# Optimization experiments

Hardware: AMD Instinct MI355X
Metric: run time of the kernel (lower is better)

Reference implementation:

```python
import jax, jax.numpy as jnp
import numpy as np
import math


def setup_inputs() -> dict:
    key = jax.random.key(0)
    k_x, k_q, k_k, k_v, k_o = jax.random.split(key, 5)
    B, S, D_IN, H, D_K, D_V, D_OUT = 1, 4096, 512, 8, 64, 64, 512
    # torch.rand -> uniform[0,1); scaled by 0.02 to keep softmax unsaturated
    scale = 0.02
    return {
        "x": jax.random.normal(k_x, (B, S, D_IN), dtype=jnp.float32),
        "W_q": jax.random.uniform(k_q, (H, D_IN, D_K), dtype=jnp.float32) * scale,
        "W_k": jax.random.uniform(k_k, (H, D_IN, D_K), dtype=jnp.float32) * scale,
        "W_v": jax.random.uniform(k_v, (H, D_IN, D_V), dtype=jnp.float32) * scale,
        "W_o": jax.random.uniform(k_o, (H, D_V, D_OUT), dtype=jnp.float32) * scale,
    }


def reference(x, W_q, W_k, W_v, W_o):
    # x: [B,S,d_in]; W_q/W_k: [H,d_in,d_k]; W_v: [H,d_in,d_v]; W_o: [H,d_v,d_out]
    S = x.shape[-2]
    d_key = W_k.shape[-1]
    Q = jnp.einsum('hjk,blj->bhlk', W_q, x)   # [B,H,S,d_k]
    K = jnp.einsum('hjk,blj->bhlk', W_k, x)   # [B,H,S,d_k]
    V = jnp.einsum('hjk,blj->bhlk', W_v, x)   # [B,H,S,d_v]
    # causal mask: True where masked (strict upper triangle)
    mask = jnp.triu(jnp.ones((S, S), dtype=bool), k=1)  # [S,S]
    scores = jnp.einsum('bhik,bhjk->bhij', Q, K)        # [B,H,S,S]
    scores = jnp.where(mask, -jnp.inf, scores)
    # is_scaled=True: divide by sqrt(d_key) before softmax
    weights = jax.nn.softmax(scores / math.sqrt(d_key), axis=-1)
    weights = jnp.where(mask, 0.0, weights)
    values = jnp.einsum('bhij,bhjv->bhiv', weights, V)  # [B,H,S,d_v]
    return jnp.einsum('hvk,bhlv->blk', W_o, values)     # [B,S,d_out]
```

## Files before the change

kernel.cpp:

```cpp
#include <hip/hip_runtime.h>
#include <hip/hip_bf16.h>
#include <math.h>

#define S_LEN 4096
#define NH    8

typedef __attribute__((ext_vector_type(8))) short bf16x8;
typedef __attribute__((ext_vector_type(4))) short bf16x4;
typedef __attribute__((ext_vector_type(4))) float f32x4;
typedef __attribute__((ext_vector_type(16))) float f32x16;
typedef __attribute__((ext_vector_type(2)))  int   int32x2;
typedef __attribute__((ext_vector_type(4)))  unsigned short u16x4;

#define QSCALE 0.18033688011112042f

#define WAIT_VM6 0x0F76
#define WAIT_VM4 0x0F74
#define WAIT_VM0 0x0F70

__device__ __forceinline__ short f2bf(float f) {
    union { float f; unsigned u; } v; v.f = f;
    unsigned r = v.u + 0x7fffu + ((v.u >> 16) & 1u);
    return (short)(r >> 16);
}

__device__ __forceinline__ float bf2f(unsigned short s) {
    union { unsigned u; float f; } v; v.u = ((unsigned)s) << 16; return v.f;
}

__device__ __forceinline__ int pk2(float a, float b) {
    __hip_bfloat162 t = __float22bfloat162_rn(make_float2(a, b));
    union { __hip_bfloat162 h; int i; } u; u.h = t;
    return u.i;
}

__device__ __forceinline__ void gload16(const void* g, void* l) {
    __builtin_amdgcn_global_load_lds(
        (const __attribute__((address_space(1))) unsigned*)g,
        (__attribute__((address_space(3))) unsigned*)l, 16, 0, 0);
}

__device__ __forceinline__ void stage_tile(const short* gsrc, size_t gstride,
                                           short* tile, int t)
{
    const int wave = t >> 6, lane = t & 63;
    const int sub = lane >> 3;
    const int cg  = (lane & 7) ^ sub;
#pragma unroll
    for (int j = 0; j < 2; ++j) {
        const int chunk = wave * 2 + j;
        const int row = chunk * 8 + sub;
        gload16(gsrc + (size_t)row * gstride + cg * 8, tile + chunk * 512);
    }
}

__device__ __forceinline__ bf16x8 frag(const short* tile, int row, int cg) {
    return *(const bf16x8*)&tile[row * 64 + ((cg ^ (row & 7)) << 3)];
}

__device__ __forceinline__ bf16x8 mk_bp(const f32x16& sc, const int p, float& lsum)
{
    const float e0 = __builtin_amdgcn_exp2f(sc[8 * p + 0]);
    const float e1 = __builtin_amdgcn_exp2f(sc[8 * p + 1]);
    const float e2 = __builtin_amdgcn_exp2f(sc[8 * p + 2]);
    const float e3 = __builtin_amdgcn_exp2f(sc[8 * p + 3]);
    const float e4 = __builtin_amdgcn_exp2f(sc[8 * p + 4]);
    const float e5 = __builtin_amdgcn_exp2f(sc[8 * p + 5]);
    const float e6 = __builtin_amdgcn_exp2f(sc[8 * p + 6]);
    const float e7 = __builtin_amdgcn_exp2f(sc[8 * p + 7]);
    lsum += ((e0 + e1) + (e2 + e3)) + ((e4 + e5) + (e6 + e7));
    int we0 = pk2(e0, e1), we1 = pk2(e2, e3);
    int wo0 = pk2(e4, e5), wo1 = pk2(e6, e7);
    const int32x2 r0 = __builtin_amdgcn_permlane32_swap(we0, wo0, false, false);
    const int32x2 r1 = __builtin_amdgcn_permlane32_swap(we1, wo1, false, false);
    union { int i[4]; bf16x8 v; } u;
    u.i[0] = r0[0]; u.i[1] = r1[0]; u.i[2] = r0[1]; u.i[3] = r1[1];
    return u.v;
}

__device__ __forceinline__ void gemm_mainloop_512(
    const short* __restrict__ Arow, const short* __restrict__ Brow,
    short* As, short* Bs, f32x4 acc[4], int t)
{
    const int wave = t >> 6, lane = t & 63, n16 = lane & 15, quad = lane >> 4;
    stage_tile(Arow, 512, As, t);
    stage_tile(Brow, 512, Bs, t);
    for (int c = 0; c < 8; ++c) {
        const int cur = c & 1;
        __builtin_amdgcn_s_barrier();
        if (c < 7) {
            stage_tile(Arow + (c + 1) * 64, 512, As + (1 - cur) * 4096, t);
            stage_tile(Brow + (c + 1) * 64, 512, Bs + (1 - cur) * 4096, t);
            __builtin_amdgcn_s_waitcnt(WAIT_VM4);
        } else {
            __builtin_amdgcn_s_waitcnt(WAIT_VM0);
        }
        __builtin_amdgcn_s_barrier();
        const short* as = As + cur * 4096;
        const short* bs = Bs + cur * 4096;
#pragma unroll
        for (int kh = 0; kh < 2; ++kh) {
            const bf16x8 a = frag(as, wave * 16 + n16, kh * 4 + quad);
#pragma unroll
            for (int nt = 0; nt < 4; ++nt) {
                const bf16x8 b = frag(bs, nt * 16 + n16, kh * 4 + quad);
                acc[nt] = __builtin_amdgcn_mfma_f32_16x16x32_bf16(a, b, acc[nt], 0, 0, 0);
            }
        }
    }
}

__global__ __launch_bounds__(256) void prep_kernel(
    const float* __restrict__ x,
    const float* __restrict__ Wq, const float* __restrict__ Wk,
    const float* __restrict__ Wv, const float* __restrict__ Wo,
    short* __restrict__ xb, short* __restrict__ Wqkvt, short* __restrict__ Wot)
{
    __shared__ short T[64 * 66];
    const int b = blockIdx.x, t = threadIdx.x;
    if (b < 1024) {
        const size_t idx = (size_t)b * 2048 + t * 8;
        const float4 a = *(const float4*)&x[idx];
        const float4 c = *(const float4*)&x[idx + 4];
        bf16x8 o;
        o[0] = f2bf(a.x); o[1] = f2bf(a.y); o[2] = f2bf(a.z); o[3] = f2bf(a.w);
        o[4] = f2bf(c.x); o[5] = f2bf(c.y); o[6] = f2bf(c.z); o[7] = f2bf(c.w);
        *(bf16x8*)&xb[idx] = o;
        return;
    }
    const int c4 = (t & 15) * 4, rsub = t >> 4;
    const int orow = t >> 2, oc16 = (t & 3) * 16;
    if (b < 1216) {
        const int jj = b - 1024, g = jj >> 3, kb = jj & 7;
        const int which = g >> 3, h = g & 7;
        const float* W = ((which == 0) ? Wq : (which == 1) ? Wk : Wv) + (size_t)h * 512 * 64;
#pragma unroll
        for (int p = 0; p < 4; ++p) {
            const int row = p * 16 + rsub;
            const float4 v = *(const float4*)&W[(size_t)(kb * 64 + row) * 64 + c4];
            T[(c4 + 0) * 66 + row] = f2bf(v.x);
            T[(c4 + 1) * 66 + row] = f2bf(v.y);
            T[(c4 + 2) * 66 + row] = f2bf(v.z);
            T[(c4 + 3) * 66 + row] = f2bf(v.w);
        }
        __syncthreads();
        short* O = &Wqkvt[((size_t)g * 64 + orow) * 512 + kb * 64];
        *(bf16x8*)&O[oc16]     = *(const bf16x8*)&T[orow * 66 + oc16];
        *(bf16x8*)&O[oc16 + 8] = *(const bf16x8*)&T[orow * 66 + oc16 + 8];
    } else {
        const int jj = b - 1216, h = jj >> 3, nb = jj & 7;
        const float* W = Wo + (size_t)h * 64 * 512;
#pragma unroll
        for (int p = 0; p < 4; ++p) {
            const int row = p * 16 + rsub;
            const float4 v = *(const float4*)&W[(size_t)row * 512 + nb * 64 + c4];
            T[(c4 + 0) * 66 + row] = f2bf(v.x);
            T[(c4 + 1) * 66 + row] = f2bf(v.y);
            T[(c4 + 2) * 66 + row] = f2bf(v.z);
            T[(c4 + 3) * 66 + row] = f2bf(v.w);
        }
        __syncthreads();
        short* O = &Wot[((size_t)nb * 64 + orow) * 512 + h * 64];
        *(bf16x8*)&O[oc16]     = *(const bf16x8*)&T[orow * 66 + oc16];
        *(bf16x8*)&O[oc16 + 8] = *(const bf16x8*)&T[orow * 66 + oc16 + 8];
    }
}

__global__ __launch_bounds__(256) void qkv_gemm_kernel(
    const short* __restrict__ xb, const short* __restrict__ Wqkvt,
    short* __restrict__ Qg, short* __restrict__ Kg, short* __restrict__ Vtg)
{
    __shared__ short smem[24576];
    short* As = smem;
    short* Bs = smem + 16384;
    const int sblk = blockIdx.x, g = blockIdx.y;
    const int which = g >> 3, h = g & 7;
    const int t = threadIdx.x;
    const int wave = t >> 6, lane = t & 63, n16 = lane & 15, quad = lane >> 4;

    const short* Arow = xb + (size_t)sblk * 128 * 512;
    const short* Brow = Wqkvt + (size_t)g * 64 * 512;

    f32x4 acc[2][4] = {{{0,0,0,0},{0,0,0,0},{0,0,0,0},{0,0,0,0}},
                       {{0,0,0,0},{0,0,0,0},{0,0,0,0},{0,0,0,0}}};

    stage_tile(Arow,            512, As,        t);
    stage_tile(Arow + 64 * 512, 512, As + 4096, t);
    stage_tile(Brow,            512, Bs,        t);
    for (int c = 0; c < 8; ++c) {
        const int cur = c & 1;
        __builtin_amdgcn_s_barrier();
        if (c < 7) {
            stage_tile(Arow + (c + 1) * 64,            512, As + (1 - cur) * 8192,        t);
            stage_tile(Arow + 64 * 512 + (c + 1) * 64, 512, As + (1 - cur) * 8192 + 4096, t);
            stage_tile(Brow + (c + 1) * 64,            512, Bs + (1 - cur) * 4096,        t);
            __builtin_amdgcn_s_waitcnt(WAIT_VM6);
        } else {
            __builtin_amdgcn_s_waitcnt(WAIT_VM0);
        }
        __builtin_amdgcn_s_barrier();
        const short* as = As + cur * 8192;
        const short* bs = Bs + cur * 4096;
        const int r0 = wave * 32 + n16;
        const short* a_sub = as + (r0 >> 6) * 4096;
#pragma unroll
        for (int kh = 0; kh < 2; ++kh) {
            const bf16x8 a0 = frag(a_sub, r0 & 63,        kh * 4 + quad);
            const bf16x8 a1 = frag(a_sub, (r0 & 63) + 16, kh * 4 + quad);
#pragma unroll
            for (int nt = 0; nt < 4; ++nt) {
                const bf16x8 b = frag(bs, nt * 16 + n16, kh * 4 + quad);
                acc[0][nt] = __builtin_amdgcn_mfma_f32_16x16x32_bf16(a0, b, acc[0][nt], 0, 0, 0);
                acc[1][nt] = __builtin_amdgcn_mfma_f32_16x16x32_bf16(a1, b, acc[1][nt], 0, 0, 0);
            }
        }
    }

    if (which < 2) {
        const float scale = (which == 0) ? QSCALE : 1.0f;
        short* O = ((which == 0) ? Qg : Kg) + (size_t)h * S_LEN * 64;
#pragma unroll
        for (int m = 0; m < 2; ++m)
#pragma unroll
            for (int nt = 0; nt < 4; ++nt)
#pragma unroll
                for (int r = 0; r < 4; ++r) {
                    const int s = sblk * 128 + wave * 32 + m * 16 + quad * 4 + r;
                    O[(size_t)s * 64 + nt * 16 + n16] = f2bf(acc[m][nt][r] * scale);
                }
    } else {
        __syncthreads();
        short* Tr = smem;
#pragma unroll
        for (int m = 0; m < 2; ++m)
#pragma unroll
            for (int nt = 0; nt < 4; ++nt)
#pragma unroll
                for (int r = 0; r < 4; ++r)
                    Tr[(nt * 16 + n16) * 130 + wave * 32 + m * 16 + quad * 4 + r] =
                        f2bf(acc[m][nt][r]);
        __syncthreads();
        short* O = Vtg + (size_t)h * 64 * S_LEN + sblk * 128;
        const int vr = t >> 2, c32 = (t & 3) * 32;
#pragma unroll
        for (int u = 0; u < 4; ++u)
            *(bf16x8*)&O[(size_t)vr * S_LEN + c32 + u * 8] =
                *(const bf16x8*)&Tr[vr * 130 + c32 + u * 8];
    }
}

__global__ __launch_bounds__(256) void out_gemm_kernel(
    const short* __restrict__ vals, const short* __restrict__ Wot, float* __restrict__ out)
{
    __shared__ short smem[16384];
    short* As = smem;
    short* Bs = smem + 8192;
    const int sblk = blockIdx.x, g = blockIdx.y;
    const int t = threadIdx.x;
    const int wave = t >> 6, lane = t & 63, n16 = lane & 15, quad = lane >> 4;

    f32x4 acc[4] = {{0,0,0,0},{0,0,0,0},{0,0,0,0},{0,0,0,0}};
    gemm_mainloop_512(vals + (size_t)sblk * 64 * 512, Wot + (size_t)g * 64 * 512,
                      As, Bs, acc, t);

#pragma unroll
    for (int nt = 0; nt < 4; ++nt)
#pragma unroll
        for (int r = 0; r < 4; ++r) {
            const int s = sblk * 64 + wave * 16 + quad * 4 + r;
            out[(size_t)s * 512 + g * 64 + nt * 16 + n16] = acc[nt][r];
        }
}

__global__ __launch_bounds__(256, 3) void attn_kernel(
    const short* __restrict__ Qg, const short* __restrict__ Kg,
    const short* __restrict__ Vtg, short* __restrict__ Opart, float* __restrict__ Lpart)
{
    __shared__ short Ks[2][4096];
    __shared__ short Vs[2][4096];

    const int id = blockIdx.x;
    const int h  = id & 7;
    const int c  = 79 - (id >> 3);
    int qs, j;
    if (c < 8)       { qs = c;                   j = 0; }
    else if (c < 24) { qs = 8 + ((c - 8) >> 1);  j = (c - 8) & 1; }
    else if (c < 48) { qs = 16 + (c - 24) / 3;   j = (c - 24) % 3; }
    else             { qs = 24 + ((c - 48) >> 2); j = (c - 48) & 3; }
    const int k0   = j * 16;
    const int kend = min(k0 + 16, 2 * qs + 2);

    const short* Kh  = Kg  + (size_t)h * S_LEN * 64;
    const short* Vth = Vtg + (size_t)h * 64 * S_LEN;

    const int t = threadIdx.x;
    const int wave = t >> 6, lane = t & 63, l31 = lane & 31, half = lane >> 5;
    const int qg = qs * 128 + wave * 32 + l31;

    const short* Qr = Qg + (size_t)h * S_LEN * 64 + (size_t)qg * 64;
    bf16x8 bq[4];
#pragma unroll
    for (int kc = 0; kc < 4; ++kc)
        bq[kc] = *(const bf16x8*)&Qr[kc * 16 + half * 8];

    f32x16 z16;
#pragma unroll
    for (int r = 0; r < 16; ++r) z16[r] = 0.f;

    f32x16 oacc[2];
#pragma unroll
    for (int r = 0; r < 16; ++r) { oacc[0][r] = 0.f; oacc[1][r] = 0.f; }
    float llane = 0.f;

    stage_tile(Kh + (size_t)k0 * 64 * 64, 64, Ks[0], t);
    stage_tile(Vth + k0 * 64, S_LEN, Vs[0], t);

    for (int kb = k0; kb < kend; ++kb) {
        const int cur = (kb - k0) & 1;
        __builtin_amdgcn_s_barrier();
        if (kb + 1 < kend) {
            stage_tile(Kh + (size_t)(kb + 1) * 64 * 64, 64, Ks[1 - cur], t);
            stage_tile(Vth + (kb + 1) * 64, S_LEN, Vs[1 - cur], t);
            __builtin_amdgcn_s_waitcnt(WAIT_VM4);
        } else {
            __builtin_amdgcn_s_waitcnt(WAIT_VM0);
        }
        __builtin_amdgcn_s_barrier();

        __builtin_amdgcn_s_setprio(1);
        f32x16 sc0, sc1;
        {
            const bf16x8 a0 = frag(Ks[cur], l31,      half);
            const bf16x8 a1 = frag(Ks[cur], 32 + l31, half);
            sc0 = __builtin_amdgcn_mfma_f32_32x32x16_bf16(a0, bq[0], z16, 0, 0, 0);
            sc1 = __builtin_amdgcn_mfma_f32_32x32x16_bf16(a1, bq[0], z16, 0, 0, 0);
        }
#pragma unroll
        for (int kc = 1; kc < 4; ++kc) {
            const bf16x8 a0 = frag(Ks[cur], l31,      kc * 2 + half);
            const bf16x8 a1 = frag(Ks[cur], 32 + l31, kc * 2 + half);
            sc0 = __builtin_amdgcn_mfma_f32_32x32x16_bf16(a0, bq[kc], sc0, 0, 0, 0);
            sc1 = __builtin_amdgcn_mfma_f32_32x32x16_bf16(a1, bq[kc], sc1, 0, 0, 0);
        }
        __builtin_amdgcn_s_setprio(0);

        if (kb * 64 + 63 > qg) {
#pragma unroll
            for (int r = 0; r < 16; ++r) {
                const int keyb = kb * 64 + (r & 3) + 8 * (r >> 2) + 4 * half;
                if (keyb > qg)      sc0[r] = -1e30f;
                if (keyb + 32 > qg) sc1[r] = -1e30f;
            }
        }

        bf16x8 bp[4];
        bp[0] = mk_bp(sc0, 0, llane);
        bp[1] = mk_bp(sc0, 1, llane);
        bp[2] = mk_bp(sc1, 0, llane);
        bp[3] = mk_bp(sc1, 1, llane);

        __builtin_amdgcn_s_setprio(1);
#pragma unroll
        for (int kc = 0; kc < 4; ++kc) {
            const bf16x8 a0 = frag(Vs[cur], l31,      kc * 2 + half);
            const bf16x8 a1 = frag(Vs[cur], 32 + l31, kc * 2 + half);
            oacc[0] = __builtin_amdgcn_mfma_f32_32x32x16_bf16(a0, bp[kc], oacc[0], 0, 0, 0);
            oacc[1] = __builtin_amdgcn_mfma_f32_32x32x16_bf16(a1, bp[kc], oacc[1], 0, 0, 0);
        }
        __builtin_amdgcn_s_setprio(0);
    }

    short* tileO = Opart + (size_t)(h * 80 + c) * (64 * 128);
    float* tileL = Lpart + (h * 80 + c) * 128;
    const float lq = llane + __shfl_xor(llane, 32, 64);
    if (half == 0) tileL[wave * 32 + l31] = lq;
#pragma unroll
    for (int mt = 0; mt < 2; ++mt)
#pragma unroll
        for (int r = 0; r < 16; ++r) {
            const int v = mt * 32 + (r & 3) + 8 * (r >> 2) + 4 * half;
            tileO[(v << 7) + wave * 32 + l31] = f2bf(mt ? oacc[1][r] : oacc[0][r]);
        }
}

__global__ __launch_bounds__(256) void combine_norm_kernel(
    const short* __restrict__ Opart, const float* __restrict__ Lpart,
    short* __restrict__ vals)
{
    __shared__ short T[128 * 66];
    const int id = blockIdx.x;
    const int h = id & 7, qs = id >> 3;
    int c0, nj;
    if (qs < 8)       { c0 = qs;                 nj = 1; }
    else if (qs < 16) { c0 = 8 + 2 * (qs - 8);   nj = 2; }
    else if (qs < 24) { c0 = 24 + 3 * (qs - 16); nj = 3; }
    else              { c0 = 48 + 4 * (qs - 24); nj = 4; }
    const int base = h * 80 + c0;

    const int t = threadIdx.x;
    const int q0 = (t & 31) * 4;
    const int vr = t >> 5;

    f32x4 L = {0, 0, 0, 0};
    for (int j = 0; j < nj; ++j)
        L += *(const f32x4*)&Lpart[(base + j) * 128 + q0];
    const f32x4 inv = {1.f / L[0], 1.f / L[1], 1.f / L[2], 1.f / L[3]};

#pragma unroll
    for (int pass = 0; pass < 8; ++pass) {
        const int v = vr + pass * 8;
        f32x4 s = {0, 0, 0, 0};
        for (int j = 0; j < nj; ++j) {
            const u16x4 u = *(const u16x4*)&Opart[(size_t)(base + j) * 8192 + (v << 7) + q0];
            s[0] += bf2f(u[0]); s[1] += bf2f(u[1]);
            s[2] += bf2f(u[2]); s[3] += bf2f(u[3]);
        }
        T[(q0 + 0) * 66 + v] = f2bf(s[0] * inv[0]);
        T[(q0 + 1) * 66 + v] = f2bf(s[1] * inv[1]);
        T[(q0 + 2) * 66 + v] = f2bf(s[2] * inv[2]);
        T[(q0 + 3) * 66 + v] = f2bf(s[3] * inv[3]);
    }
    __syncthreads();
    const int q = t >> 1, vh = (t & 1) * 32;
    const size_t row = (size_t)(qs * 128 + q) * 512 + h * 64 + vh;
#pragma unroll
    for (int u = 0; u < 4; ++u)
        *(bf16x8*)&vals[row + u * 8] = *(const bf16x8*)&T[q * 66 + vh + u * 8];
}

extern "C" void kernel_launch(void* const* d_in, const int* in_sizes, int n_in,
                              void* d_out, int out_size, void* d_ws, size_t ws_size,
                              hipStream_t stream)
{
    const float* x  = (const float*)d_in[0];
    const float* Wq = (const float*)d_in[1];
    const float* Wk = (const float*)d_in[2];
    const float* Wv = (const float*)d_in[3];
    const float* Wo = (const float*)d_in[4];
    float* out = (float*)d_out;

    short* xb    = (short*)d_ws;
    short* Wqkvt = xb + 2097152;
    short* Wot   = Wqkvt + 786432;
    short* Qg    = Wot + 262144;
    short* Kg    = Qg + 2097152;
    short* Vtg   = Kg + 2097152;
    short* vals  = Vtg + 2097152;
    short* Opart = vals + 2097152;
    float* Lpart = (float*)(Opart + (size_t)640 * 8192);

    prep_kernel<<<1280, 256, 0, stream>>>(x, Wq, Wk, Wv, Wo, xb, Wqkvt, Wot);
    qkv_gemm_kernel<<<dim3(32, 24), 256, 0, stream>>>(xb, Wqkvt, Qg, Kg, Vtg);
    attn_kernel<<<640, 256, 0, stream>>>(Qg, Kg, Vtg, Opart, Lpart);
    combine_norm_kernel<<<256, 256, 0, stream>>>(Opart, Lpart, vals);
    out_gemm_kernel<<<dim3(64, 8), 256, 0, stream>>>(vals, Wot, out);
}
```

Before: 135.2 us.

## Fuse all five stages into one cooperative persistent kernel with grid syncs

Folds the prep, QKV GEMM, attention, combine and output GEMM stages into one cooperative kernel of 768 blocks, separated by grid-wide barriers. If the cooperative launch fails it falls back to the original five launches. The aim is to remove four kernel launch gaps and tails. In exchange, every stage now runs with the fused kernel's register and occupancy limits (launch_bounds 256,3), and grid.sync adds its own barrier cost.

```diff
diff --git a/kernel.cpp b/kernel.cpp
--- a/kernel.cpp
+++ b/kernel.cpp
@@ -1,4 +1,5 @@
 #include <hip/hip_runtime.h>
+#include <hip/hip_cooperative_groups.h>
 #include <hip/hip_bf16.h>
 #include <math.h>
 
@@ -110,14 +111,13 @@
     }
 }
 
-__global__ __launch_bounds__(256) void prep_kernel(
+__device__ __forceinline__ void prep_body(
+    int b, int t, short* T,
     const float* __restrict__ x,
     const float* __restrict__ Wq, const float* __restrict__ Wk,
     const float* __restrict__ Wv, const float* __restrict__ Wo,
     short* __restrict__ xb, short* __restrict__ Wqkvt, short* __restrict__ Wot)
 {
-    __shared__ short T[64 * 66];
-    const int b = blockIdx.x, t = threadIdx.x;
     if (b < 1024) {
         const size_t idx = (size_t)b * 2048 + t * 8;
         const float4 a = *(const float4*)&x[idx];
@@ -166,16 +166,14 @@
     }
 }
 
-__global__ __launch_bounds__(256) void qkv_gemm_kernel(
+__device__ __forceinline__ void qkv_body(
+    int sblk, int g, int t, short* smem,
     const short* __restrict__ xb, const short* __restrict__ Wqkvt,
     short* __restrict__ Qg, short* __restrict__ Kg, short* __restrict__ Vtg)
 {
-    __shared__ short smem[24576];
     short* As = smem;
     short* Bs = smem + 16384;
-    const int sblk = blockIdx.x, g = blockIdx.y;
     const int which = g >> 3, h = g & 7;
-    const int t = threadIdx.x;
     const int wave = t >> 6, lane = t & 63, n16 = lane & 15, quad = lane >> 4;
 
     const short* Arow = xb + (size_t)sblk * 128 * 512;
@@ -249,37 +247,12 @@
     }
 }
 
-__global__ __launch_bounds__(256) void out_gemm_kernel(
-    const short* __restrict__ vals, const short* __restrict__ Wot, float* __restrict__ out)
-{
-    __shared__ short smem[16384];
-    short* As = smem;
-    short* Bs = smem + 8192;
-    const int sblk = blockIdx.x, g = blockIdx.y;
-    const int t = threadIdx.x;
-    const int wave = t >> 6, lane = t & 63, n16 = lane & 15, quad = lane >> 4;
-
-    f32x4 acc[4] = {{0,0,0,0},{0,0,0,0},{0,0,0,0},{0,0,0,0}};
-    gemm_mainloop_512(vals + (size_t)sblk * 64 * 512, Wot + (size_t)g * 64 * 512,
-                      As, Bs, acc, t);
-
-#pragma unroll
-    for (int nt = 0; nt < 4; ++nt)
-#pragma unroll
-        for (int r = 0; r < 4; ++r) {
-            const int s = sblk * 64 + wave * 16 + quad * 4 + r;
-            out[(size_t)s * 512 + g * 64 + nt * 16 + n16] = acc[nt][r];
-        }
-}
-
-__global__ __launch_bounds__(256, 3) void attn_kernel(
+__device__ __forceinline__ void attn_body(
+    int id, int t, short* smem,
     const short* __restrict__ Qg, const short* __restrict__ Kg,
-    const short* __restrict__ Vtg, short* __restrict__ Opart, float* __restrict__ Lpart)
-{
-    __shared__ short Ks[2][4096];
-    __shared__ short Vs[2][4096];
-
-    const int id = blockIdx.x;
+    const short* __restrict__ Vtg, short* __restrict__ Opart,
+    float* __restrict__ Lpart)
+{
     const int h  = id & 7;
     const int c  = 79 - (id >> 3);
     int qs, j;
@@ -293,7 +266,6 @@
     const short* Kh  = Kg  + (size_t)h * S_LEN * 64;
     const short* Vth = Vtg + (size_t)h * 64 * S_LEN;
 
-    const int t = threadIdx.x;
     const int wave = t >> 6, lane = t & 63, l31 = lane & 31, half = lane >> 5;
     const int qg = qs * 128 + wave * 32 + l31;
 
@@ -312,15 +284,17 @@
     for (int r = 0; r < 16; ++r) { oacc[0][r] = 0.f; oacc[1][r] = 0.f; }
     float llane = 0.f;
 
-    stage_tile(Kh + (size_t)k0 * 64 * 64, 64, Ks[0], t);
-    stage_tile(Vth + k0 * 64, S_LEN, Vs[0], t);
+    stage_tile(Kh + (size_t)k0 * 64 * 64, 64, smem, t);
+    stage_tile(Vth + k0 * 64, S_LEN, smem + 8192, t);
 
     for (int kb = k0; kb < kend; ++kb) {
         const int cur = (kb - k0) & 1;
+        const short* Kc = smem + cur * 4096;
+        const short* Vc = smem + 8192 + cur * 4096;
         __builtin_amdgcn_s_barrier();
         if (kb + 1 < kend) {
-            stage_tile(Kh + (size_t)(kb + 1) * 64 * 64, 64, Ks[1 - cur], t);
-            stage_tile(Vth + (kb + 1) * 64, S_LEN, Vs[1 - cur], t);
+            stage_tile(Kh + (size_t)(kb + 1) * 64 * 64, 64, smem + (1 - cur) * 4096, t);
+            stage_tile(Vth + (kb + 1) * 64, S_LEN, smem + 8192 + (1 - cur) * 4096, t);
             __builtin_amdgcn_s_waitcnt(WAIT_VM4);
         } else {
             __builtin_amdgcn_s_waitcnt(WAIT_VM0);
@@ -330,15 +304,15 @@
         __builtin_amdgcn_s_setprio(1);
         f32x16 sc0, sc1;
         {
-            const bf16x8 a0 = frag(Ks[cur], l31,      half);
-            const bf16x8 a1 = frag(Ks[cur], 32 + l31, half);
+            const bf16x8 a0 = frag(Kc, l31,      half);
+            const bf16x8 a1 = frag(Kc, 32 + l31, half);
             sc0 = __builtin_amdgcn_mfma_f32_32x32x16_bf16(a0, bq[0], z16, 0, 0, 0);
             sc1 = __builtin_amdgcn_mfma_f32_32x32x16_bf16(a1, bq[0], z16, 0, 0, 0);
         }
 #pragma unroll
         for (int kc = 1; kc < 4; ++kc) {
-            const bf16x8 a0 = frag(Ks[cur], l31,      kc * 2 + half);
-            const bf16x8 a1 = frag(Ks[cur], 32 + l31, kc * 2 + half);
+            const bf16x8 a0 = frag(Kc, l31,      kc * 2 + half);
+            const bf16x8 a1 = frag(Kc, 32 + l31, kc * 2 + half);
             sc0 = __builtin_amdgcn_mfma_f32_32x32x16_bf16(a0, bq[kc], sc0, 0, 0, 0);
             sc1 = __builtin_amdgcn_mfma_f32_32x32x16_bf16(a1, bq[kc], sc1, 0, 0, 0);
         }
@@ -362,8 +336,8 @@
         __builtin_amdgcn_s_setprio(1);
 #pragma unroll
         for (int kc = 0; kc < 4; ++kc) {
-            const bf16x8 a0 = frag(Vs[cur], l31,      kc * 2 + half);
-            const bf16x8 a1 = frag(Vs[cur], 32 + l31, kc * 2 + half);
+            const bf16x8 a0 = frag(Vc, l31,      kc * 2 + half);
+            const bf16x8 a1 = frag(Vc, 32 + l31, kc * 2 + half);
             oacc[0] = __builtin_amdgcn_mfma_f32_32x32x16_bf16(a0, bp[kc], oacc[0], 0, 0, 0);
             oacc[1] = __builtin_amdgcn_mfma_f32_32x32x16_bf16(a1, bp[kc], oacc[1], 0, 0, 0);
         }
@@ -383,12 +357,11 @@
         }
 }
 
-__global__ __launch_bounds__(256) void combine_norm_kernel(
+__device__ __forceinline__ void combine_body(
+    int id, int t, short* T,
     const short* __restrict__ Opart, const float* __restrict__ Lpart,
     short* __restrict__ vals)
 {
-    __shared__ short T[128 * 66];
-    const int id = blockIdx.x;
     const int h = id & 7, qs = id >> 3;
     int c0, nj;
     if (qs < 8)       { c0 = qs;                 nj = 1; }
@@ -397,7 +370,6 @@
     else              { c0 = 48 + 4 * (qs - 24); nj = 4; }
     const int base = h * 80 + c0;
 
-    const int t = threadIdx.x;
     const int q0 = (t & 31) * 4;
     const int vr = t >> 5;
 
@@ -426,6 +398,98 @@
 #pragma unroll
     for (int u = 0; u < 4; ++u)
         *(bf16x8*)&vals[row + u * 8] = *(const bf16x8*)&T[q * 66 + vh + u * 8];
+}
+
+__device__ __forceinline__ void out_body(
+    int sblk, int g, int t, short* smem,
+    const short* __restrict__ vals, const short* __restrict__ Wot,
+    float* __restrict__ out)
+{
+    short* As = smem;
+    short* Bs = smem + 8192;
+    const int wave = t >> 6, lane = t & 63, n16 = lane & 15, quad = lane >> 4;
+
+    f32x4 acc[4] = {{0,0,0,0},{0,0,0,0},{0,0,0,0},{0,0,0,0}};
+    gemm_mainloop_512(vals + (size_t)sblk * 64 * 512, Wot + (size_t)g * 64 * 512,
+                      As, Bs, acc, t);
+
+#pragma unroll
+    for (int nt = 0; nt < 4; ++nt)
+#pragma unroll
+        for (int r = 0; r < 4; ++r) {
+            const int s = sblk * 64 + wave * 16 + quad * 4 + r;
+            out[(size_t)s * 512 + g * 64 + nt * 16 + n16] = acc[nt][r];
+        }
+}
+
+__global__ __launch_bounds__(256, 3) void fused_kernel(
+    const float* __restrict__ x,
+    const float* __restrict__ Wq, const float* __restrict__ Wk,
+    const float* __restrict__ Wv, const float* __restrict__ Wo,
+    float* __restrict__ out,
+    short* __restrict__ xb, short* __restrict__ Wqkvt, short* __restrict__ Wot,
+    short* __restrict__ Qg, short* __restrict__ Kg, short* __restrict__ Vtg,
+    short* __restrict__ vals, short* __restrict__ Opart, float* __restrict__ Lpart)
+{
+    cooperative_groups::grid_group grid = cooperative_groups::this_grid();
+    __shared__ short smem[24576];
+    const int bid = blockIdx.x, t = threadIdx.x;
+
+    for (int u = bid; u < 1280; u += 768)
+        prep_body(u, t, smem, x, Wq, Wk, Wv, Wo, xb, Wqkvt, Wot);
+    grid.sync();
+
+    qkv_body(bid & 31, bid >> 5, t, smem, xb, Wqkvt, Qg, Kg, Vtg);
+    grid.sync();
+
+    if (bid < 640) attn_body(bid, t, smem, Qg, Kg, Vtg, Opart, Lpart);
+    grid.sync();
+
+    if (bid < 256) combine_body(bid, t, smem, Opart, Lpart, vals);
+    grid.sync();
+
+    if (bid < 512) out_body(bid & 63, bid >> 6, t, smem, vals, Wot, out);
+}
+
+__global__ __launch_bounds__(256) void prep_kernel(
+    const float* __restrict__ x,
+    const float* __restrict__ Wq, const float* __restrict__ Wk,
+    const float* __restrict__ Wv, const float* __restrict__ Wo,
+    short* __restrict__ xb, short* __restrict__ Wqkvt, short* __restrict__ Wot)
+{
+    __shared__ short T[64 * 66];
+    prep_body(blockIdx.x, threadIdx.x, T, x, Wq, Wk, Wv, Wo, xb, Wqkvt, Wot);
+}
+
+__global__ __launch_bounds__(256) void qkv_gemm_kernel(
+    const short* __restrict__ xb, const short* __restrict__ Wqkvt,
+    short* __restrict__ Qg, short* __restrict__ Kg, short* __restrict__ Vtg)
+{
+    __shared__ short smem[24576];
+    qkv_body(blockIdx.x, blockIdx.y, threadIdx.x, smem, xb, Wqkvt, Qg, Kg, Vtg);
+}
+
+__global__ __launch_bounds__(256, 3) void attn_kernel(
+    const short* __restrict__ Qg, const short* __restrict__ Kg,
+    const short* __restrict__ Vtg, short* __restrict__ Opart, float* __restrict__ Lpart)
+{
+    __shared__ short smem[16384];
+    attn_body(blockIdx.x, threadIdx.x, smem, Qg, Kg, Vtg, Opart, Lpart);
+}
+
+__global__ __launch_bounds__(256) void combine_norm_kernel(
+    const short* __restrict__ Opart, const float* __restrict__ Lpart,
+    short* __restrict__ vals)
+{
+    __shared__ short T[128 * 66];
+    combine_body(blockIdx.x, threadIdx.x, T, Opart, Lpart, vals);
+}
+
+__global__ __launch_bounds__(256) void out_gemm_kernel(
+    const short* __restrict__ vals, const short* __restrict__ Wot, float* __restrict__ out)
+{
+    __shared__ short smem[16384];
+    out_body(blockIdx.x, blockIdx.y, threadIdx.x, smem, vals, Wot, out);
 }
 
 extern "C" void kernel_launch(void* const* d_in, const int* in_sizes, int n_in,
@@ -449,9 +513,18 @@
     short* Opart = vals + 2097152;
     float* Lpart = (float*)(Opart + (size_t)640 * 8192);
 
-    prep_kernel<<<1280, 256, 0, stream>>>(x, Wq, Wk, Wv, Wo, xb, Wqkvt, Wot);
-    qkv_gemm_kernel<<<dim3(32, 24), 256, 0, stream>>>(xb, Wqkvt, Qg, Kg, Vtg);
-    attn_kernel<<<640, 256, 0, stream>>>(Qg, Kg, Vtg, Opart, Lpart);
-    combine_norm_kernel<<<256, 256, 0, stream>>>(Opart, Lpart, vals);
-    out_gemm_kernel<<<dim3(64, 8), 256, 0, stream>>>(vals, Wot, out);
-}
+    void* args[] = {(void*)&x, (void*)&Wq, (void*)&Wk, (void*)&Wv, (void*)&Wo,
+                    (void*)&out, (void*)&xb, (void*)&Wqkvt, (void*)&Wot,
+                    (void*)&Qg, (void*)&Kg, (void*)&Vtg, (void*)&vals,
+                    (void*)&Opart, (void*)&Lpart};
+    const hipError_t e = hipLaunchCooperativeKernel(
+        (void*)fused_kernel, dim3(768), dim3(256), args, 0, stream);
+    if (e != hipSuccess) {
+        (void)hipGetLastError();
+        prep_kernel<<<1280, 256, 0, stream>>>(x, Wq, Wk, Wv, Wo, xb, Wqkvt, Wot);
+        qkv_gemm_kernel<<<dim3(32, 24), 256, 0, stream>>>(xb, Wqkvt, Qg, Kg, Vtg);
+        attn_kernel<<<640, 256, 0, stream>>>(Qg, Kg, Vtg, Opart, Lpart);
+        combine_norm_kernel<<<256, 256, 0, stream>>>(Opart, Lpart, vals);
+        out_gemm_kernel<<<dim3(64, 8), 256, 0, stream>>>(vals, Wot, out);
+    }
+}
```

After: 509.2 us. 3.77x slower.
